# Kernel optimization log

Hardware: AMD Instinct MI355X
Metric: run time of the kernel (lower is better)

## Reference

```python
import math
import jax, jax.numpy as jnp
import numpy as np

BASE_MASK_PROB = 0.15
ENTROPY_TARGET = 0.7
MIN_ACTIVE = 1
EPS = 1e-8
NEG_LOG_EPS = -math.log(1e-8)

B, H, S = 4, 16, 1024


def setup_inputs() -> dict:
    key = jax.random.key(0)
    k1, k2 = jax.random.split(key)
    weights = jax.random.uniform(k1, (B, H, S, S), dtype=jnp.float32)
    # uniform noise replaces torch.bernoulli: mask = (noise < keep_prob)
    noise = jax.random.uniform(k2, (B, H, S, S), dtype=jnp.float32)
    return {"weights": weights, "noise": noise}


def _xlogy(x, y):
    # matches torch.xlogy: 0 * log(0) == 0
    return jnp.where(x == 0.0, 0.0, x * jnp.log(jnp.where(x == 0.0, 1.0, y)))


def reference(weights, noise):
    seq_len = weights.shape[-1]
    dtype = weights.dtype

    # normalize rows; degenerate (near-zero) rows become uniform
    weight_sums = jnp.sum(weights, axis=-1, keepdims=True)
    needs_norm = weight_sums < EPS
    safe_sums = jnp.where(needs_norm, 1.0, weight_sums)
    w = jnp.where(needs_norm, 1.0 / seq_len, weights / safe_sums)

    # fused entropy, clamped to -log(eps)
    entropy = jnp.minimum(-jnp.sum(_xlogy(w, w), axis=-1), NEG_LOG_EPS)

    max_entropy = math.log(float(seq_len))
    norm_entropy = jnp.clip(entropy / max_entropy, 0.0, 1.0)
    adaptive_prob = BASE_MASK_PROB * (1.0 - norm_entropy)
    keep_prob = 1.0 - adaptive_prob[..., None]          # [B,H,S,1]

    # bernoulli(keep_prob) via supplied uniform noise
    mask = (noise < keep_prob).astype(dtype)            # [B,H,S,S]

    # min_active fallback: rows with too few kept entries keep their top-k
    k = min(MIN_ACTIVE, seq_len)
    active_count = jnp.sum(mask, axis=-1)
    needs_more = active_count < k                        # [B,H,S]
    _, top_idx = jax.lax.top_k(w, k)                     # [B,H,S,k]
    min_mask = jnp.sum(jax.nn.one_hot(top_idx, seq_len, dtype=dtype), axis=-2)
    mask = jnp.where(needs_more[..., None], min_mask, mask)

    # mask and renormalize; fall back to unmasked weights if row sum ~ 0
    masked = w * mask
    msum = jnp.sum(masked, axis=-1, keepdims=True)
    valid = msum > EPS
    final_weights = jnp.where(valid, masked / jnp.where(valid, msum, 1.0), w)

    mask_rate = 1.0 - jnp.mean(mask, axis=-1)
    target_entropy = jnp.full_like(entropy, max_entropy * ENTROPY_TARGET)
    return final_weights, entropy, mask_rate, target_entropy
```

## Files before the change

### kernel.cpp

```cpp
#include <hip/hip_runtime.h>
#include <math.h>

namespace {
constexpr int kS = 1024;
constexpr float kEps = 1e-8f;
constexpr float kNegLogEps = 18.420680743952367f;
constexpr float kMaxEntropy = 6.9314718055994531f;
constexpr float kInvMaxEntropy = 1.0f / 6.9314718055994531f;
constexpr float kTargetEntropy = 4.8520302639196169f;
constexpr float kBaseMaskProb = 0.15f;
}

__global__ __launch_bounds__(256, 4)
void curriculum_kernel(const float* __restrict__ weights,
                       const float* __restrict__ noise,
                       float* __restrict__ out_w,
                       float* __restrict__ out_ent,
                       float* __restrict__ out_mrate,
                       float* __restrict__ out_tent,
                       int nrows)
{
    const int lane = threadIdx.x & 63;
    const int wid  = threadIdx.x >> 6;
    const int row  = blockIdx.x * 4 + wid;
    if (row >= nrows) return;

    const long long base = (long long)row * kS;
    const float4* __restrict__ wsrc = reinterpret_cast<const float4*>(weights + base);

    float w[16];
    {
        float4 a = wsrc[lane];
        float4 b = wsrc[lane + 64];
        float4 c = wsrc[lane + 128];
        float4 d = wsrc[lane + 192];
        w[0]=a.x;  w[1]=a.y;  w[2]=a.z;  w[3]=a.w;
        w[4]=b.x;  w[5]=b.y;  w[6]=b.z;  w[7]=b.w;
        w[8]=c.x;  w[9]=c.y;  w[10]=c.z; w[11]=c.w;
        w[12]=d.x; w[13]=d.y; w[14]=d.z; w[15]=d.w;
    }

    float s = ((w[0]+w[1])+(w[2]+w[3])) + ((w[4]+w[5])+(w[6]+w[7]))
            + ((w[8]+w[9])+(w[10]+w[11])) + ((w[12]+w[13])+(w[14]+w[15]));
    #pragma unroll
    for (int o = 1; o < 64; o <<= 1) s += __shfl_xor(s, o, 64);

    if (s < kEps) {
        #pragma unroll
        for (int i = 0; i < 16; ++i) w[i] = 1.0f / (float)kS;
    } else {
        const float inv = 1.0f / s;
        #pragma unroll
        for (int i = 0; i < 16; ++i) w[i] *= inv;
    }

    float ep = 0.0f;
    #pragma unroll
    for (int i = 0; i < 16; ++i)
        ep += (w[i] != 0.0f) ? w[i] * __logf(w[i]) : 0.0f;
    #pragma unroll
    for (int o = 1; o < 64; o <<= 1) ep += __shfl_xor(ep, o, 64);

    const float entropy   = fminf(-ep, kNegLogEps);
    const float nent      = fminf(fmaxf(entropy * kInvMaxEntropy, 0.0f), 1.0f);
    const float keep_prob = 1.0f - kBaseMaskProb * (1.0f - nent);

    const float4* __restrict__ nsrc = reinterpret_cast<const float4*>(noise + base);
    float nz[16];
    {
        float4 a = nsrc[lane];
        float4 b = nsrc[lane + 64];
        float4 c = nsrc[lane + 128];
        float4 d = nsrc[lane + 192];
        nz[0]=a.x;  nz[1]=a.y;  nz[2]=a.z;  nz[3]=a.w;
        nz[4]=b.x;  nz[5]=b.y;  nz[6]=b.z;  nz[7]=b.w;
        nz[8]=c.x;  nz[9]=c.y;  nz[10]=c.z; nz[11]=c.w;
        nz[12]=d.x; nz[13]=d.y; nz[14]=d.z; nz[15]=d.w;
    }

    unsigned mask = 0u;
    float msum = 0.0f;
    int cnt = 0;
    #pragma unroll
    for (int i = 0; i < 16; ++i) {
        if (nz[i] < keep_prob) { mask |= (1u << i); msum += w[i]; ++cnt; }
    }

    float mxv = w[0];
    int   mxi = lane * 4;
    #pragma unroll
    for (int i = 1; i < 16; ++i) {
        const int idx = ((i >> 2) << 8) + lane * 4 + (i & 3);
        if (w[i] > mxv) { mxv = w[i]; mxi = idx; }
    }

    #pragma unroll
    for (int o = 1; o < 64; o <<= 1) {
        cnt  += __shfl_xor(cnt,  o, 64);
        msum += __shfl_xor(msum, o, 64);
        const float ov = __shfl_xor(mxv, o, 64);
        const int   oi = __shfl_xor(mxi, o, 64);
        if (ov > mxv || (ov == mxv && oi < mxi)) { mxv = ov; mxi = oi; }
    }

    if (cnt < 1) {
        mask = (((mxi >> 2) & 63) == lane) ? (1u << (((mxi >> 8) << 2) | (mxi & 3))) : 0u;
        msum = mxv;
        cnt  = 1;
    }

    const bool  valid = msum > kEps;
    const float invm  = valid ? 1.0f / msum : 0.0f;

    float f[16];
    #pragma unroll
    for (int i = 0; i < 16; ++i) {
        const float kept = ((mask >> i) & 1u) ? w[i] * invm : 0.0f;
        f[i] = valid ? kept : w[i];
    }

    float4* __restrict__ dst = reinterpret_cast<float4*>(out_w + base);
    dst[lane]       = make_float4(f[0],  f[1],  f[2],  f[3]);
    dst[lane + 64]  = make_float4(f[4],  f[5],  f[6],  f[7]);
    dst[lane + 128] = make_float4(f[8],  f[9],  f[10], f[11]);
    dst[lane + 192] = make_float4(f[12], f[13], f[14], f[15]);

    if (lane == 0) {
        out_ent[row]   = entropy;
        out_mrate[row] = 1.0f - (float)cnt * (1.0f / (float)kS);
        out_tent[row]  = kTargetEntropy;
    }
}

extern "C" void kernel_launch(void* const* d_in, const int* in_sizes, int n_in,
                              void* d_out, int out_size, void* d_ws, size_t ws_size,
                              hipStream_t stream)
{
    (void)n_in; (void)d_ws; (void)ws_size; (void)out_size;

    const float* weights = (const float*)d_in[0];
    const float* noise   = (const float*)d_in[1];
    const long long total = (long long)in_sizes[0];
    const int nrows = (int)(total / kS);

    float* out_w     = (float*)d_out;
    float* out_ent   = out_w + total;
    float* out_mrate = out_ent + nrows;
    float* out_tent  = out_mrate + nrows;

    const int blocks = (nrows + 3) / 4;
    hipLaunchKernelGGL(curriculum_kernel, dim3(blocks), dim3(256), 0, stream,
                       weights, noise, out_w, out_ent, out_mrate, out_tent, nrows);
}
```

Measured before the change: 148.8 us.

## Hoist noise loads, fuse sum and entropy reductions, use nontemporal stores

Issues the noise loads together with the weight loads so all memory traffic for a row is in flight at once. Computes the row sum and the unnormalized w*log(w) in a single pass, then derives entropy algebraically as log(s) - p/s. The argmax reduction now runs only when no element in the row is kept. Output stores become nontemporal, and the launch-bounds occupancy hint rises to 8. The algebraic entropy form and the rescaled validity check can differ slightly from the reference numerically.

```diff
diff --git a/kernel.cpp b/kernel.cpp
--- a/kernel.cpp
+++ b/kernel.cpp
@@ -9,9 +9,10 @@
 constexpr float kInvMaxEntropy = 1.0f / 6.9314718055994531f;
 constexpr float kTargetEntropy = 4.8520302639196169f;
 constexpr float kBaseMaskProb = 0.15f;
+typedef float f32x4 __attribute__((ext_vector_type(4)));
 }
 
-__global__ __launch_bounds__(256, 4)
+__global__ __launch_bounds__(256, 8)
 void curriculum_kernel(const float* __restrict__ weights,
                        const float* __restrict__ noise,
                        float* __restrict__ out_w,
@@ -27,109 +28,108 @@
 
     const long long base = (long long)row * kS;
     const float4* __restrict__ wsrc = reinterpret_cast<const float4*>(weights + base);
+    const float4* __restrict__ nsrc = reinterpret_cast<const float4*>(noise + base);
+
+    float4 a0 = wsrc[lane];
+    float4 a1 = wsrc[lane + 64];
+    float4 a2 = wsrc[lane + 128];
+    float4 a3 = wsrc[lane + 192];
+    float4 b0 = nsrc[lane];
+    float4 b1 = nsrc[lane + 64];
+    float4 b2 = nsrc[lane + 128];
+    float4 b3 = nsrc[lane + 192];
 
     float w[16];
-    {
-        float4 a = wsrc[lane];
-        float4 b = wsrc[lane + 64];
-        float4 c = wsrc[lane + 128];
-        float4 d = wsrc[lane + 192];
-        w[0]=a.x;  w[1]=a.y;  w[2]=a.z;  w[3]=a.w;
-        w[4]=b.x;  w[5]=b.y;  w[6]=b.z;  w[7]=b.w;
-        w[8]=c.x;  w[9]=c.y;  w[10]=c.z; w[11]=c.w;
-        w[12]=d.x; w[13]=d.y; w[14]=d.z; w[15]=d.w;
+    w[0]=a0.x;  w[1]=a0.y;  w[2]=a0.z;  w[3]=a0.w;
+    w[4]=a1.x;  w[5]=a1.y;  w[6]=a1.z;  w[7]=a1.w;
+    w[8]=a2.x;  w[9]=a2.y;  w[10]=a2.z; w[11]=a2.w;
+    w[12]=a3.x; w[13]=a3.y; w[14]=a3.z; w[15]=a3.w;
+
+    float s = 0.0f, p = 0.0f;
+    #pragma unroll
+    for (int i = 0; i < 16; ++i) {
+        s += w[i];
+        p += w[i] * __logf(fmaxf(w[i], 1e-37f));
     }
 
-    float s = ((w[0]+w[1])+(w[2]+w[3])) + ((w[4]+w[5])+(w[6]+w[7]))
-            + ((w[8]+w[9])+(w[10]+w[11])) + ((w[12]+w[13])+(w[14]+w[15]));
     #pragma unroll
-    for (int o = 1; o < 64; o <<= 1) s += __shfl_xor(s, o, 64);
+    for (int o = 1; o < 64; o <<= 1) {
+        s += __shfl_xor(s, o, 64);
+        p += __shfl_xor(p, o, 64);
+    }
 
     if (s < kEps) {
         #pragma unroll
         for (int i = 0; i < 16; ++i) w[i] = 1.0f / (float)kS;
-    } else {
-        const float inv = 1.0f / s;
-        #pragma unroll
-        for (int i = 0; i < 16; ++i) w[i] *= inv;
+        s = 1.0f;
+        p = -kMaxEntropy;
     }
 
-    float ep = 0.0f;
+    const float inv_s   = 1.0f / s;
+    const float entropy = fminf(__logf(s) - p * inv_s, kNegLogEps);
+    const float nent    = fminf(fmaxf(entropy * kInvMaxEntropy, 0.0f), 1.0f);
+    const float keep    = 1.0f - kBaseMaskProb * (1.0f - nent);
+
+    float nz[16];
+    nz[0]=b0.x;  nz[1]=b0.y;  nz[2]=b0.z;  nz[3]=b0.w;
+    nz[4]=b1.x;  nz[5]=b1.y;  nz[6]=b1.z;  nz[7]=b1.w;
+    nz[8]=b2.x;  nz[9]=b2.y;  nz[10]=b2.z; nz[11]=b2.w;
+    nz[12]=b3.x; nz[13]=b3.y; nz[14]=b3.z; nz[15]=b3.w;
+
+    unsigned mask = 0u;
+    float msum = 0.0f, cntf = 0.0f;
     #pragma unroll
-    for (int i = 0; i < 16; ++i)
-        ep += (w[i] != 0.0f) ? w[i] * __logf(w[i]) : 0.0f;
-    #pragma unroll
-    for (int o = 1; o < 64; o <<= 1) ep += __shfl_xor(ep, o, 64);
-
-    const float entropy   = fminf(-ep, kNegLogEps);
-    const float nent      = fminf(fmaxf(entropy * kInvMaxEntropy, 0.0f), 1.0f);
-    const float keep_prob = 1.0f - kBaseMaskProb * (1.0f - nent);
-
-    const float4* __restrict__ nsrc = reinterpret_cast<const float4*>(noise + base);
-    float nz[16];
-    {
-        float4 a = nsrc[lane];
-        float4 b = nsrc[lane + 64];
-        float4 c = nsrc[lane + 128];
-        float4 d = nsrc[lane + 192];
-        nz[0]=a.x;  nz[1]=a.y;  nz[2]=a.z;  nz[3]=a.w;
-        nz[4]=b.x;  nz[5]=b.y;  nz[6]=b.z;  nz[7]=b.w;
-        nz[8]=c.x;  nz[9]=c.y;  nz[10]=c.z; nz[11]=c.w;
-        nz[12]=d.x; nz[13]=d.y; nz[14]=d.z; nz[15]=d.w;
+    for (int i = 0; i < 16; ++i) {
+        if (nz[i] < keep) { mask |= (1u << i); msum += w[i]; cntf += 1.0f; }
     }
 
-    unsigned mask = 0u;
-    float msum = 0.0f;
-    int cnt = 0;
-    #pragma unroll
-    for (int i = 0; i < 16; ++i) {
-        if (nz[i] < keep_prob) { mask |= (1u << i); msum += w[i]; ++cnt; }
-    }
-
-    float mxv = w[0];
-    int   mxi = lane * 4;
-    #pragma unroll
-    for (int i = 1; i < 16; ++i) {
-        const int idx = ((i >> 2) << 8) + lane * 4 + (i & 3);
-        if (w[i] > mxv) { mxv = w[i]; mxi = idx; }
-    }
+    const unsigned long long anyk = __ballot(mask != 0u);
 
     #pragma unroll
     for (int o = 1; o < 64; o <<= 1) {
-        cnt  += __shfl_xor(cnt,  o, 64);
+        cntf += __shfl_xor(cntf, o, 64);
         msum += __shfl_xor(msum, o, 64);
-        const float ov = __shfl_xor(mxv, o, 64);
-        const int   oi = __shfl_xor(mxi, o, 64);
-        if (ov > mxv || (ov == mxv && oi < mxi)) { mxv = ov; mxi = oi; }
     }
 
-    if (cnt < 1) {
+    if (anyk == 0ull) {
+        float mxv = w[0];
+        int   mxi = lane * 4;
+        #pragma unroll
+        for (int i = 1; i < 16; ++i) {
+            const int idx = ((i >> 2) << 8) + lane * 4 + (i & 3);
+            if (w[i] > mxv) { mxv = w[i]; mxi = idx; }
+        }
+        #pragma unroll
+        for (int o = 1; o < 64; o <<= 1) {
+            const float ov = __shfl_xor(mxv, o, 64);
+            const int   oi = __shfl_xor(mxi, o, 64);
+            if (ov > mxv || (ov == mxv && oi < mxi)) { mxv = ov; mxi = oi; }
+        }
         mask = (((mxi >> 2) & 63) == lane) ? (1u << (((mxi >> 8) << 2) | (mxi & 3))) : 0u;
         msum = mxv;
-        cnt  = 1;
+        cntf = 1.0f;
     }
 
-    const bool  valid = msum > kEps;
-    const float invm  = valid ? 1.0f / msum : 0.0f;
+    const bool  valid = msum > kEps * s;
+    const float scale = valid ? 1.0f / msum : inv_s;
 
-    float f[16];
+    f32x4 f0, f1, f2, f3;
     #pragma unroll
     for (int i = 0; i < 16; ++i) {
-        const float kept = ((mask >> i) & 1u) ? w[i] * invm : 0.0f;
-        f[i] = valid ? kept : w[i];
+        const float v = (valid && !((mask >> i) & 1u)) ? 0.0f : w[i] * scale;
+        f32x4* dstv = (i < 4) ? &f0 : (i < 8) ? &f1 : (i < 12) ? &f2 : &f3;
+        (*dstv)[i & 3] = v;
     }
 
-    float4* __restrict__ dst = reinterpret_cast<float4*>(out_w + base);
-    dst[lane]       = make_float4(f[0],  f[1],  f[2],  f[3]);
-    dst[lane + 64]  = make_float4(f[4],  f[5],  f[6],  f[7]);
-    dst[lane + 128] = make_float4(f[8],  f[9],  f[10], f[11]);
-    dst[lane + 192] = make_float4(f[12], f[13], f[14], f[15]);
+    f32x4* __restrict__ dst = reinterpret_cast<f32x4*>(out_w + base);
+    __builtin_nontemporal_store(f0, dst + lane);
+    __builtin_nontemporal_store(f1, dst + lane + 64);
+    __builtin_nontemporal_store(f2, dst + lane + 128);
+    __builtin_nontemporal_store(f3, dst + lane + 192);
 
-    if (lane == 0) {
-        out_ent[row]   = entropy;
-        out_mrate[row] = 1.0f - (float)cnt * (1.0f / (float)kS);
-        out_tent[row]  = kTargetEntropy;
-    }
+    if (lane == 0) out_ent[row]   = entropy;
+    if (lane == 1) out_mrate[row] = 1.0f - cntf * (1.0f / (float)kS);
+    if (lane == 2) out_tent[row]  = kTargetEntropy;
 }
 
 extern "C" void kernel_launch(void* const* d_in, const int* in_sizes, int n_in,
```

Result: faster. 143.4 us (-3.6%).
